# Performance work log

Measured on AMD Instinct MI355X. Metric: run time of the kernel, lower is better.

Reference implementation:

```python
import jax, jax.numpy as jnp
import numpy as np

N = 100000      # nodes
E = 1600000     # edges (avg degree 16)
F_IN = 128
F_OUT = 128
EPS = 1e-5      # BatchNorm eps


def setup_inputs() -> dict:
    key = jax.random.key(0)
    ks = jax.random.split(key, 10)
    s_in = 1.0 / np.sqrt(F_IN)
    s_out = 1.0 / np.sqrt(F_OUT)
    return {
        "x": jax.random.normal(ks[0], (N, F_IN), dtype=jnp.float32),
        "edge_index": jax.random.randint(ks[1], (2, E), 0, N, dtype=jnp.int32),
        # layer 0: SAGEConv(F_IN, F_OUT, aggr='max'); lin_l has bias, lin_r does not
        "W0_l": jax.random.normal(ks[2], (F_IN, F_OUT), dtype=jnp.float32) * s_in,
        "b0_l": jnp.zeros((F_OUT,), dtype=jnp.float32),
        "W0_r": jax.random.normal(ks[3], (F_IN, F_OUT), dtype=jnp.float32) * s_in,
        "gamma0": jnp.ones((F_OUT,), dtype=jnp.float32),
        "beta0": jnp.zeros((F_OUT,), dtype=jnp.float32),
        # layer 1: SAGEConv(F_OUT, F_OUT, aggr='max')
        "W1_l": jax.random.normal(ks[4], (F_OUT, F_OUT), dtype=jnp.float32) * s_out,
        "b1_l": jnp.zeros((F_OUT,), dtype=jnp.float32),
        "W1_r": jax.random.normal(ks[5], (F_OUT, F_OUT), dtype=jnp.float32) * s_out,
        "gamma1": jnp.ones((F_OUT,), dtype=jnp.float32),
        "beta1": jnp.zeros((F_OUT,), dtype=jnp.float32),
    }


def _sage_conv_max(x, src, dst, W_l, b_l, W_r):
    # gather source features along edges, scatter-max into destination nodes
    msgs = x[src]                                             # [E, F]
    agg = jax.ops.segment_max(msgs, dst, num_segments=N)      # [N, F], -inf for isolated
    agg = jnp.where(jnp.isfinite(agg), agg, 0.0)              # PyG fills empty segments with 0
    return agg @ W_l + b_l + x @ W_r                          # lin_l(aggr) + lin_r(x)


def _batch_norm(h, gamma, beta):
    mu = jnp.mean(h, axis=0)
    var = jnp.var(h, axis=0)
    return (h - mu) * jax.lax.rsqrt(var + EPS) * gamma + beta


def reference(x, edge_index, W0_l, b0_l, W0_r, gamma0, beta0,
              W1_l, b1_l, W1_r, gamma1, beta1):
    src, dst = edge_index[0], edge_index[1]
    h = _sage_conv_max(x, src, dst, W0_l, b0_l, W0_r)
    h = jax.nn.relu(_batch_norm(h, gamma0, beta0))
    h = _sage_conv_max(h, src, dst, W1_l, b1_l, W1_r)
    h = jax.nn.relu(_batch_norm(h, gamma1, beta1))
    return h
```

## Files before the change

kernel.cpp:

```cpp
#include <hip/hip_runtime.h>
#include <stdint.h>

#define EPS_BN 1e-5f

typedef __attribute__((ext_vector_type(8))) short short8v;
typedef __attribute__((ext_vector_type(4))) float f32x4;

__device__ __forceinline__ unsigned rne_bf16(float f) {
    unsigned u = __float_as_uint(f);
    return (u + 0x7FFFu + ((u >> 16) & 1u)) >> 16;
}

extern "C" __global__ __launch_bounds__(256)
void prep_kernel(const float4* __restrict__ x, uint2* __restrict__ x16, long n4, int cvB,
                 const float* __restrict__ Wl0, const float* __restrict__ Wr0,
                 unsigned short* __restrict__ Wt0,
                 const float* __restrict__ Wl1, const float* __restrict__ Wr1,
                 unsigned short* __restrict__ Wt1,
                 int* __restrict__ head, int Nn) {
    int b = blockIdx.x;
    if (b < cvB) {
        long i = (long)b * 256 + threadIdx.x;
        long stride = (long)cvB * 256;
        for (; i < n4; i += stride) {
            float4 v = x[i];
            uint2 o;
            o.x = rne_bf16(v.x) | (rne_bf16(v.y) << 16);
            o.y = rne_bf16(v.z) | (rne_bf16(v.w) << 16);
            x16[i] = o;
        }
    } else if (b < cvB + 256) {
        int wb = b - cvB;
        const float* Wl = (wb < 128) ? Wl0 : Wl1;
        const float* Wr = (wb < 128) ? Wr0 : Wr1;
        unsigned short* Wt = (wb < 128) ? Wt0 : Wt1;
        int idx = (wb & 127) * 256 + threadIdx.x;
        int col = idx >> 8, k = idx & 255;
        float v = (k < 128) ? Wl[(size_t)k * 128 + col]
                            : Wr[(size_t)(k - 128) * 128 + col];
        Wt[(size_t)col * 256 + k] = (unsigned short)rne_bf16(v);
    } else {
        int i = (b - cvB - 256) * 256 + threadIdx.x;
        if (i < Nn) head[i] = -1;
    }
}

extern "C" __global__ __launch_bounds__(256)
void link_kernel(const int* __restrict__ ei, int* __restrict__ head,
                 uint2* __restrict__ pair, int E) {
    int e = blockIdx.x * 256 + threadIdx.x;
    if (e < E) {
        int src = ei[e];
        int dst = ei[E + e];
        int old = atomicExch(&head[dst], e);
        uint2 p; p.x = (unsigned)src; p.y = (unsigned)old;
        pair[e] = p;
    }
}

extern "C" __global__ __launch_bounds__(256, 8)
void gather_max_ll16_kernel(const uint4* __restrict__ x16r, const int* __restrict__ head,
                            const uint2* __restrict__ pair,
                            uint4* __restrict__ agg16, float* __restrict__ stats, int Nn) {
    if (blockIdx.x == 0 && threadIdx.x < 256) stats[threadIdx.x] = 0.0f;
    int t = blockIdx.x * 256 + threadIdx.x;
    int node = t >> 4;
    if (node >= Nn) return;
    int lane = t & 15;
    int e = head[node];
    uint4 out;
    if (e >= 0) {
        uint2 p = pair[e];
        uint4 r = x16r[(size_t)p.x * 16 + lane];
        float a0 = __uint_as_float(r.x << 16), a1 = __uint_as_float(r.x);
        float a2 = __uint_as_float(r.y << 16), a3 = __uint_as_float(r.y);
        float a4 = __uint_as_float(r.z << 16), a5 = __uint_as_float(r.z);
        float a6 = __uint_as_float(r.w << 16), a7 = __uint_as_float(r.w);
        int en = (int)p.y;
        while (en >= 0) {
            uint2 pn = pair[en];
            uint4 v = x16r[(size_t)pn.x * 16 + lane];
            en = (int)pn.y;
            a0 = fmaxf(a0, __uint_as_float(v.x << 16));
            a1 = fmaxf(a1, __uint_as_float(v.x));
            a2 = fmaxf(a2, __uint_as_float(v.y << 16));
            a3 = fmaxf(a3, __uint_as_float(v.y));
            a4 = fmaxf(a4, __uint_as_float(v.z << 16));
            a5 = fmaxf(a5, __uint_as_float(v.z));
            a6 = fmaxf(a6, __uint_as_float(v.w << 16));
            a7 = fmaxf(a7, __uint_as_float(v.w));
        }
        out.x = (__float_as_uint(a0) >> 16) | (__float_as_uint(a1) & 0xFFFF0000u);
        out.y = (__float_as_uint(a2) >> 16) | (__float_as_uint(a3) & 0xFFFF0000u);
        out.z = (__float_as_uint(a4) >> 16) | (__float_as_uint(a5) & 0xFFFF0000u);
        out.w = (__float_as_uint(a6) >> 16) | (__float_as_uint(a7) & 0xFFFF0000u);
    } else {
        out.x = out.y = out.z = out.w = 0u;
    }
    agg16[(size_t)node * 16 + lane] = out;
}

extern "C" __global__ __launch_bounds__(256, 8)
void gather_max_bn_kernel(const uint4* __restrict__ h1r, const int* __restrict__ head,
                          const uint2* __restrict__ pair,
                          const float* __restrict__ stats0,
                          const float* __restrict__ gamma, const float* __restrict__ beta,
                          float inv_n,
                          uint4* __restrict__ agg16, uint4* __restrict__ y16,
                          float* __restrict__ stats1, int Nn) {
    __shared__ float scT[8][17];
    __shared__ float shT[8][17];
    {
        int t = threadIdx.x;
        if (t < 128) {
            float mu = stats0[t] * inv_n;
            float var = stats0[128 + t] * inv_n - mu * mu;
            float sc = gamma[t] * rsqrtf(var + EPS_BN);
            scT[t & 7][t >> 3] = sc;
            shT[t & 7][t >> 3] = beta[t] - mu * sc;
        }
        __syncthreads();
    }
    if (blockIdx.x == 0 && threadIdx.x < 256) stats1[threadIdx.x] = 0.0f;

    int t = blockIdx.x * 256 + threadIdx.x;
    int node = t >> 4;
    if (node >= Nn) return;
    int lane = t & 15;

    float sc[8], sh[8];
#pragma unroll
    for (int j = 0; j < 8; ++j) {
        sc[j] = scT[j][lane];
        sh[j] = shT[j][lane];
    }

    {
        uint4 r = h1r[(size_t)node * 16 + lane];
        float v0 = __uint_as_float(r.x << 16), v1 = __uint_as_float(r.x & 0xFFFF0000u);
        float v2 = __uint_as_float(r.y << 16), v3 = __uint_as_float(r.y & 0xFFFF0000u);
        float v4 = __uint_as_float(r.z << 16), v5 = __uint_as_float(r.z & 0xFFFF0000u);
        float v6 = __uint_as_float(r.w << 16), v7 = __uint_as_float(r.w & 0xFFFF0000u);
        v0 = fmaxf(fmaf(v0, sc[0], sh[0]), 0.f);
        v1 = fmaxf(fmaf(v1, sc[1], sh[1]), 0.f);
        v2 = fmaxf(fmaf(v2, sc[2], sh[2]), 0.f);
        v3 = fmaxf(fmaf(v3, sc[3], sh[3]), 0.f);
        v4 = fmaxf(fmaf(v4, sc[4], sh[4]), 0.f);
        v5 = fmaxf(fmaf(v5, sc[5], sh[5]), 0.f);
        v6 = fmaxf(fmaf(v6, sc[6], sh[6]), 0.f);
        v7 = fmaxf(fmaf(v7, sc[7], sh[7]), 0.f);
        uint4 o;
        o.x = rne_bf16(v0) | (rne_bf16(v1) << 16);
        o.y = rne_bf16(v2) | (rne_bf16(v3) << 16);
        o.z = rne_bf16(v4) | (rne_bf16(v5) << 16);
        o.w = rne_bf16(v6) | (rne_bf16(v7) << 16);
        y16[(size_t)node * 16 + lane] = o;
    }

    int e = head[node];
    uint4 out;
    if (e >= 0) {
        uint2 p = pair[e];
        uint4 r = h1r[(size_t)p.x * 16 + lane];
        float a0 = __uint_as_float(r.x << 16), a1 = __uint_as_float(r.x);
        float a2 = __uint_as_float(r.y << 16), a3 = __uint_as_float(r.y);
        float a4 = __uint_as_float(r.z << 16), a5 = __uint_as_float(r.z);
        float a6 = __uint_as_float(r.w << 16), a7 = __uint_as_float(r.w);
        int en = (int)p.y;
        while (en >= 0) {
            uint2 pn = pair[en];
            uint4 v = h1r[(size_t)pn.x * 16 + lane];
            en = (int)pn.y;
            a0 = fmaxf(a0, __uint_as_float(v.x << 16));
            a1 = fmaxf(a1, __uint_as_float(v.x));
            a2 = fmaxf(a2, __uint_as_float(v.y << 16));
            a3 = fmaxf(a3, __uint_as_float(v.y));
            a4 = fmaxf(a4, __uint_as_float(v.z << 16));
            a5 = fmaxf(a5, __uint_as_float(v.z));
            a6 = fmaxf(a6, __uint_as_float(v.w << 16));
            a7 = fmaxf(a7, __uint_as_float(v.w));
        }
        a1 = __uint_as_float(__float_as_uint(a1) & 0xFFFF0000u);
        a3 = __uint_as_float(__float_as_uint(a3) & 0xFFFF0000u);
        a5 = __uint_as_float(__float_as_uint(a5) & 0xFFFF0000u);
        a7 = __uint_as_float(__float_as_uint(a7) & 0xFFFF0000u);
        a0 = fmaxf(fmaf(a0, sc[0], sh[0]), 0.f);
        a1 = fmaxf(fmaf(a1, sc[1], sh[1]), 0.f);
        a2 = fmaxf(fmaf(a2, sc[2], sh[2]), 0.f);
        a3 = fmaxf(fmaf(a3, sc[3], sh[3]), 0.f);
        a4 = fmaxf(fmaf(a4, sc[4], sh[4]), 0.f);
        a5 = fmaxf(fmaf(a5, sc[5], sh[5]), 0.f);
        a6 = fmaxf(fmaf(a6, sc[6], sh[6]), 0.f);
        a7 = fmaxf(fmaf(a7, sc[7], sh[7]), 0.f);
        out.x = rne_bf16(a0) | (rne_bf16(a1) << 16);
        out.y = rne_bf16(a2) | (rne_bf16(a3) << 16);
        out.z = rne_bf16(a4) | (rne_bf16(a5) << 16);
        out.w = rne_bf16(a6) | (rne_bf16(a7) << 16);
    } else {
        out.x = out.y = out.z = out.w = 0u;
    }
    agg16[(size_t)node * 16 + lane] = out;
}

template <int OUT_BF16>
__device__ __forceinline__
void gemm_bf16_body(const unsigned short* __restrict__ agg16,
                    const unsigned short* __restrict__ xin16,
                    const unsigned short* __restrict__ Wt,
                    const float* __restrict__ bias,
                    void* __restrict__ hout, float* __restrict__ stats, int nrows) {
    __shared__ float redS[4][128];
    __shared__ float redQ[4][128];

    const int t = threadIdx.x;
    const int w = t >> 6, l = t & 63;
    const int wm = w >> 1, wn = w & 1;
    const int r16 = l & 15, g = l >> 4;
    const int blockRow = blockIdx.x * 128;
    const int colBase = wn * 64;

    f32x4 acc[4][4];
#pragma unroll
    for (int m = 0; m < 4; ++m)
#pragma unroll
        for (int n = 0; n < 4; ++n) acc[m][n] = (f32x4){0.f, 0.f, 0.f, 0.f};

    const short8v az = {0, 0, 0, 0, 0, 0, 0, 0};

#pragma unroll
    for (int kt = 0; kt < 8; ++kt) {
        const unsigned short* Asrc = (kt < 4) ? agg16 : xin16;
        const int kofs = (kt < 4) ? kt * 32 : kt * 32 - 128;

        short8v b[4];
#pragma unroll
        for (int n = 0; n < 4; ++n) {
            int col = colBase + n * 16 + r16;
            b[n] = *(const short8v*)(Wt + (size_t)col * 256 + kt * 32 + g * 8);
        }
        short8v a[4];
#pragma unroll
        for (int m = 0; m < 4; ++m) {
            int row = blockRow + wm * 64 + m * 16 + r16;
            a[m] = (row < nrows)
                 ? *(const short8v*)(Asrc + (size_t)row * 128 + kofs + g * 8)
                 : az;
        }
#pragma unroll
        for (int m = 0; m < 4; ++m)
#pragma unroll
            for (int n = 0; n < 4; ++n)
                acc[m][n] = __builtin_amdgcn_mfma_f32_16x16x32_bf16(a[m], b[n], acc[m][n], 0, 0, 0);
    }

    for (int i = t; i < 512; i += 256) {
        ((float*)redS)[i] = 0.f;
        ((float*)redQ)[i] = 0.f;
    }
    __syncthreads();

    float bcol[4];
#pragma unroll
    for (int n = 0; n < 4; ++n) bcol[n] = bias[colBase + n * 16 + r16];

    float s4[4] = {0.f, 0.f, 0.f, 0.f};
    float q4[4] = {0.f, 0.f, 0.f, 0.f};
#pragma unroll
    for (int m = 0; m < 4; ++m) {
#pragma unroll
        for (int reg = 0; reg < 4; ++reg) {
            int row = blockRow + wm * 64 + m * 16 + g * 4 + reg;
            if (row < nrows) {
#pragma unroll
                for (int n = 0; n < 4; ++n) {
                    float o = acc[m][n][reg] + bcol[n];
                    int col = colBase + n * 16 + r16;
                    if (OUT_BF16)
                        ((unsigned short*)hout)[(size_t)row * 128 + col] =
                            (unsigned short)rne_bf16(o);
                    else
                        ((float*)hout)[(size_t)row * 128 + col] = o;
                    s4[n] += o;
                    q4[n] += o * o;
                }
            }
        }
    }
#pragma unroll
    for (int n = 0; n < 4; ++n) {
        s4[n] += __shfl_xor(s4[n], 16, 64);
        s4[n] += __shfl_xor(s4[n], 32, 64);
        q4[n] += __shfl_xor(q4[n], 16, 64);
        q4[n] += __shfl_xor(q4[n], 32, 64);
    }
    if (g == 0) {
#pragma unroll
        for (int n = 0; n < 4; ++n) {
            redS[w][colBase + n * 16 + r16] = s4[n];
            redQ[w][colBase + n * 16 + r16] = q4[n];
        }
    }
    __syncthreads();
    if (t < 128) {
        float s = redS[0][t] + redS[1][t] + redS[2][t] + redS[3][t];
        float q = redQ[0][t] + redQ[1][t] + redQ[2][t] + redQ[3][t];
        atomicAdd(&stats[t], s);
        atomicAdd(&stats[128 + t], q);
    }
}

extern "C" __global__ __launch_bounds__(256)
void gemm_bf16_out16_kernel(const unsigned short* __restrict__ agg16,
                            const unsigned short* __restrict__ xin16,
                            const unsigned short* __restrict__ Wt,
                            const float* __restrict__ bias,
                            unsigned short* __restrict__ h, float* __restrict__ stats,
                            int nrows) {
    gemm_bf16_body<1>(agg16, xin16, Wt, bias, h, stats, nrows);
}

extern "C" __global__ __launch_bounds__(256)
void gemm_bf16_out32_kernel(const unsigned short* __restrict__ agg16,
                            const unsigned short* __restrict__ xin16,
                            const unsigned short* __restrict__ Wt,
                            const float* __restrict__ bias,
                            float* __restrict__ h, float* __restrict__ stats,
                            int nrows) {
    gemm_bf16_body<0>(agg16, xin16, Wt, bias, h, stats, nrows);
}

extern "C" __global__ __launch_bounds__(256)
void bn_relu_f32_kernel(float4* __restrict__ h, const float* __restrict__ stats,
                        const float* __restrict__ gamma, const float* __restrict__ beta,
                        float inv_n, long n4) {
    __shared__ float s_ss[256];
    {
        int t = threadIdx.x;
        if (t < 128) {
            float mu = stats[t] * inv_n;
            float var = stats[128 + t] * inv_n - mu * mu;
            float sc = gamma[t] * rsqrtf(var + EPS_BN);
            s_ss[t] = sc;
            s_ss[128 + t] = beta[t] - mu * sc;
        }
        __syncthreads();
    }
    long i = (long)blockIdx.x * blockDim.x + threadIdx.x;
    long stride = (long)gridDim.x * blockDim.x;
    for (; i < n4; i += stride) {
        int c4 = (int)(i & 31) * 4;
        float4 v = h[i];
        v.x = fmaxf(fmaf(v.x, s_ss[c4 + 0], s_ss[128 + c4 + 0]), 0.f);
        v.y = fmaxf(fmaf(v.y, s_ss[c4 + 1], s_ss[128 + c4 + 1]), 0.f);
        v.z = fmaxf(fmaf(v.z, s_ss[c4 + 2], s_ss[128 + c4 + 2]), 0.f);
        v.w = fmaxf(fmaf(v.w, s_ss[c4 + 3], s_ss[128 + c4 + 3]), 0.f);
        h[i] = v;
    }
}

__device__ __forceinline__ unsigned map_f(float f) {
    unsigned u = __float_as_uint(f);
    return (u & 0x80000000u) ? ~u : (u | 0x80000000u);
}
__device__ __forceinline__ float unmap_f(unsigned m) {
    return (m & 0x80000000u) ? __uint_as_float(m & 0x7FFFFFFFu) : __uint_as_float(~m);
}

extern "C" __global__ __launch_bounds__(256)
void init_sentinel_kernel(uint4* __restrict__ agg, long n4) {
    uint4 z = {0u, 0u, 0u, 0u};
    long i = (long)blockIdx.x * blockDim.x + threadIdx.x;
    long stride = (long)gridDim.x * blockDim.x;
    for (; i < n4; i += stride) agg[i] = z;
}

extern "C" __global__ __launch_bounds__(256)
void scatter_max_kernel(const float4* __restrict__ xin, const int* __restrict__ ei,
                        unsigned* __restrict__ agg, int E) {
    int t = blockIdx.x * 256 + threadIdx.x;
    int e = t >> 5;
    if (e >= E) return;
    int f4 = t & 31;
    int src = ei[e];
    int dst = ei[E + e];
    float4 v = xin[(size_t)src * 32 + f4];
    unsigned* p = agg + (size_t)dst * 128 + (size_t)f4 * 4;
    atomicMax(p + 0, map_f(v.x));
    atomicMax(p + 1, map_f(v.y));
    atomicMax(p + 2, map_f(v.z));
    atomicMax(p + 3, map_f(v.w));
}

extern "C" __global__ __launch_bounds__(256)
void unmap_kernel(unsigned* __restrict__ agg, long n) {
    long i = (long)blockIdx.x * blockDim.x + threadIdx.x;
    long stride = (long)gridDim.x * blockDim.x;
    for (; i < n; i += stride) {
        unsigned u = agg[i];
        agg[i] = __float_as_uint(u ? unmap_f(u) : 0.0f);
    }
}

extern "C" __global__
void zero_stats_kernel(float* __restrict__ stats) {
    stats[threadIdx.x] = 0.0f;
}

extern "C" __global__ __launch_bounds__(256)
void gemm_kernel(const float* __restrict__ agg, const float* __restrict__ xin,
                 const float* __restrict__ Wl, const float* __restrict__ Wr,
                 const float* __restrict__ bias, float* __restrict__ h,
                 float* __restrict__ stats, int nrows) {
    __shared__ __align__(16) float As[64][36];
    __shared__ __align__(16) float Bs[32][136];
    __shared__ float redS[4][128];
    __shared__ float redQ[4][128];

    const int t = threadIdx.x;
    const int tx = t & 15;
    const int ty = t >> 4;
    const int tx8 = tx * 8;
    const int ty4 = ty * 4;
    const int blockRow = blockIdx.x * 64;

    float acc[4][8];
#pragma unroll
    for (int j = 0; j < 4; ++j)
#pragma unroll
        for (int c = 0; c < 8; ++c) acc[j][c] = 0.0f;

    for (int kt = 0; kt < 8; ++kt) {
        const int k0 = kt * 32;
        const bool isAgg = (kt < 4);
        const float* W = isAgg ? Wl : Wr;
        const float* Asrc = isAgg ? agg : xin;
        const int kw = isAgg ? k0 : (k0 - 128);

#pragma unroll
        for (int it = 0; it < 4; ++it) {
            int idx = t + it * 256;
            int kr = idx >> 5, cq = idx & 31;
            float4 ww = *(const float4*)&W[(size_t)(kw + kr) * 128 + cq * 4];
            *(float4*)&Bs[kr][cq * 4] = ww;
        }
#pragma unroll
        for (int it = 0; it < 2; ++it) {
            int idx = t + it * 256;
            int r = idx >> 3, kq = idx & 7;
            int row_g = blockRow + r;
            float4 a = {0.f, 0.f, 0.f, 0.f};
            if (row_g < nrows)
                a = *(const float4*)&Asrc[(size_t)row_g * 128 + kw + kq * 4];
            *(float4*)&As[r][kq * 4] = a;
        }
        __syncthreads();

#pragma unroll
        for (int kk = 0; kk < 32; ++kk) {
            float aa[4];
            aa[0] = As[ty4 + 0][kk];
            aa[1] = As[ty4 + 1][kk];
            aa[2] = As[ty4 + 2][kk];
            aa[3] = As[ty4 + 3][kk];
            float4 b0 = *(const float4*)&Bs[kk][tx8];
            float4 b1 = *(const float4*)&Bs[kk][tx8 + 4];
            float bb[8] = {b0.x, b0.y, b0.z, b0.w, b1.x, b1.y, b1.z, b1.w};
#pragma unroll
            for (int j = 0; j < 4; ++j)
#pragma unroll
                for (int c = 0; c < 8; ++c)
                    acc[j][c] = fmaf(aa[j], bb[c], acc[j][c]);
        }
        __syncthreads();
    }

    float bv[8];
#pragma unroll
    for (int c = 0; c < 8; ++c) bv[c] = bias[tx8 + c];

    float s_loc[8], q_loc[8];
#pragma unroll
    for (int c = 0; c < 8; ++c) { s_loc[c] = 0.f; q_loc[c] = 0.f; }

#pragma unroll
    for (int j = 0; j < 4; ++j) {
        int row = blockRow + ty4 + j;
        if (row < nrows) {
            float o[8];
#pragma unroll
            for (int c = 0; c < 8; ++c) {
                o[c] = acc[j][c] + bv[c];
                s_loc[c] += o[c];
                q_loc[c] += o[c] * o[c];
            }
            float4 o0 = {o[0], o[1], o[2], o[3]};
            float4 o1 = {o[4], o[5], o[6], o[7]};
            *(float4*)&h[(size_t)row * 128 + tx8] = o0;
            *(float4*)&h[(size_t)row * 128 + tx8 + 4] = o1;
        }
    }

#pragma unroll
    for (int c = 0; c < 8; ++c) {
        s_loc[c] += __shfl_xor(s_loc[c], 16, 64);
        s_loc[c] += __shfl_xor(s_loc[c], 32, 64);
        q_loc[c] += __shfl_xor(q_loc[c], 16, 64);
        q_loc[c] += __shfl_xor(q_loc[c], 32, 64);
    }
    int wave = t >> 6;
    if ((t & 63) < 16) {
#pragma unroll
        for (int c = 0; c < 8; ++c) {
            redS[wave][tx8 + c] = s_loc[c];
            redQ[wave][tx8 + c] = q_loc[c];
        }
    }
    __syncthreads();
    if (t < 128) {
        float s = redS[0][t] + redS[1][t] + redS[2][t] + redS[3][t];
        float q = redQ[0][t] + redQ[1][t] + redQ[2][t] + redQ[3][t];
        atomicAdd(&stats[t], s);
        atomicAdd(&stats[128 + t], q);
    }
}

static void run_layer_atomic(const float* in_feat, const int* ei, int Nn, int Ee,
                             const float* Wl, const float* bl, const float* Wr,
                             const float* gamma, const float* beta,
                             float* agg, float* stats, float* out, hipStream_t stream) {
    long aggN = (long)Nn * 128;
    long n4 = aggN / 4;

    zero_stats_kernel<<<1, 256, 0, stream>>>(stats);
    int initBlocks = (int)((n4 + 255) / 256);
    if (initBlocks > 4096) initBlocks = 4096;
    init_sentinel_kernel<<<initBlocks, 256, 0, stream>>>((uint4*)agg, n4);
    int sb = (int)(((long)Ee * 32 + 255) / 256);
    scatter_max_kernel<<<sb, 256, 0, stream>>>((const float4*)in_feat, ei,
                                               (unsigned*)agg, Ee);
    int ub = (int)((aggN + 255) / 256);
    if (ub > 8192) ub = 8192;
    unmap_kernel<<<ub, 256, 0, stream>>>((unsigned*)agg, aggN);
    gemm_kernel<<<(Nn + 63) / 64, 256, 0, stream>>>(agg, in_feat, Wl, Wr, bl,
                                                    out, stats, Nn);
    int bnBlocks = (int)((n4 + 255) / 256);
    if (bnBlocks > 8192) bnBlocks = 8192;
    bn_relu_f32_kernel<<<bnBlocks, 256, 0, stream>>>((float4*)out, stats, gamma, beta,
                                                     1.0f / (float)Nn, n4);
}

extern "C" void kernel_launch(void* const* d_in, const int* in_sizes, int n_in,
                              void* d_out, int out_size, void* d_ws, size_t ws_size,
                              hipStream_t stream) {
    (void)n_in; (void)out_size;
    const float* x     = (const float*)d_in[0];
    const int*   ei    = (const int*)d_in[1];
    const float* W0_l  = (const float*)d_in[2];
    const float* b0_l  = (const float*)d_in[3];
    const float* W0_r  = (const float*)d_in[4];
    const float* g0    = (const float*)d_in[5];
    const float* be0   = (const float*)d_in[6];
    const float* W1_l  = (const float*)d_in[7];
    const float* b1_l  = (const float*)d_in[8];
    const float* W1_r  = (const float*)d_in[9];
    const float* g1    = (const float*)d_in[10];
    const float* be1   = (const float*)d_in[11];

    int Nn = in_sizes[0] / 128;
    int Ee = in_sizes[1] / 2;
    long n4 = (long)Nn * 32;
    float inv_n = 1.0f / (float)Nn;

    char* p = (char*)d_ws;
    unsigned short* xy16 = (unsigned short*)p;  p += (size_t)Nn * 128 * 2;
    unsigned short* agg16 = (unsigned short*)p; p += (size_t)Nn * 128 * 2;
    float* stats0 = (float*)p;                  p += 256 * sizeof(float);
    float* stats1 = (float*)p;                  p += 256 * sizeof(float);
    unsigned short* Wt0 = (unsigned short*)p;   p += 128 * 256 * 2;
    unsigned short* Wt1 = (unsigned short*)p;   p += 128 * 256 * 2;
    int* head = (int*)p;                        p += (size_t)Nn * sizeof(int);
    uint2* pair = (uint2*)p;                    p += (size_t)Ee * sizeof(uint2);
    size_t needed = (size_t)(p - (char*)d_ws);
    float* out = (float*)d_out;
    unsigned short* h1 = (unsigned short*)d_out;

    if (ws_size >= needed) {
        int cvB = (int)((n4 + 255) / 256);
        if (cvB > 4096) cvB = 4096;
        int hB = (Nn + 255) / 256;
        prep_kernel<<<cvB + 256 + hB, 256, 0, stream>>>(
            (const float4*)x, (uint2*)xy16, n4, cvB,
            W0_l, W0_r, Wt0, W1_l, W1_r, Wt1, head, Nn);
        link_kernel<<<(Ee + 255) / 256, 256, 0, stream>>>(ei, head, pair, Ee);

        int gB = (Nn * 16 + 255) / 256;
        int mB = (Nn + 127) / 128;
        int bnB = (int)((n4 + 255) / 256);
        if (bnB > 8192) bnB = 8192;

        gather_max_ll16_kernel<<<gB, 256, 0, stream>>>(
            (const uint4*)xy16, head, pair, (uint4*)agg16, stats0, Nn);
        gemm_bf16_out16_kernel<<<mB, 256, 0, stream>>>(agg16, xy16, Wt0, b0_l,
                                                       h1, stats0, Nn);
        gather_max_bn_kernel<<<gB, 256, 0, stream>>>(
            (const uint4*)h1, head, pair, stats0, g0, be0, inv_n,
            (uint4*)agg16, (uint4*)xy16, stats1, Nn);
        gemm_bf16_out32_kernel<<<mB, 256, 0, stream>>>(agg16, xy16, Wt1, b1_l,
                                                       out, stats1, Nn);
        bn_relu_f32_kernel<<<bnB, 256, 0, stream>>>((float4*)out, stats1, g1, be1,
                                                    inv_n, n4);
    } else {
        float* agg = (float*)d_ws;
        float* fstats = (float*)((char*)d_ws + (size_t)Nn * 128 * sizeof(float));
        run_layer_atomic(x, ei, Nn, Ee, W0_l, b0_l, W0_r, g0, be0,
                         agg, fstats, out, stream);
        run_layer_atomic(out, ei, Nn, Ee, W1_l, b1_l, W1_r, g1, be1,
                         agg, fstats, out, stream);
    }
}
```

Baseline: 393.4 us.

## Build CSR via degree histogram and scan so layer-2 gather uses contiguous source lists

Adds a degree histogram in the link kernel plus a three-kernel exclusive scan to form row offsets. The first-layer gather, while walking the linked list, writes each node's source indices into a contiguous CSR array. The second-layer gather then reads contiguous indices and issues two feature loads per iteration, removing the dependent pointer chase. The cost is three extra small launches, an extra atomic per edge and extra index writes in layer one.

```diff
diff --git a/kernel.cpp b/kernel.cpp
--- a/kernel.cpp
+++ b/kernel.cpp
@@ -17,7 +17,7 @@
                  unsigned short* __restrict__ Wt0,
                  const float* __restrict__ Wl1, const float* __restrict__ Wr1,
                  unsigned short* __restrict__ Wt1,
-                 int* __restrict__ head, int Nn) {
+                 int* __restrict__ head, int* __restrict__ deg, int Nn) {
     int b = blockIdx.x;
     if (b < cvB) {
         long i = (long)b * 256 + threadIdx.x;
@@ -41,13 +41,13 @@
         Wt[(size_t)col * 256 + k] = (unsigned short)rne_bf16(v);
     } else {
         int i = (b - cvB - 256) * 256 + threadIdx.x;
-        if (i < Nn) head[i] = -1;
-    }
-}
-
-extern "C" __global__ __launch_bounds__(256)
-void link_kernel(const int* __restrict__ ei, int* __restrict__ head,
-                 uint2* __restrict__ pair, int E) {
+        if (i < Nn) { head[i] = -1; deg[i] = 0; }
+    }
+}
+
+extern "C" __global__ __launch_bounds__(256)
+void link_hist_kernel(const int* __restrict__ ei, int* __restrict__ head,
+                      uint2* __restrict__ pair, int* __restrict__ deg, int E) {
     int e = blockIdx.x * 256 + threadIdx.x;
     if (e < E) {
         int src = ei[e];
@@ -55,12 +55,85 @@
         int old = atomicExch(&head[dst], e);
         uint2 p; p.x = (unsigned)src; p.y = (unsigned)old;
         pair[e] = p;
-    }
+        atomicAdd(&deg[dst], 1);
+    }
+}
+
+extern "C" __global__ __launch_bounds__(256)
+void block_sum_kernel(const int* __restrict__ deg, int* __restrict__ bsum, int Nn) {
+    __shared__ int tsum[256];
+    int t = threadIdx.x;
+    int base = blockIdx.x * 1024 + t * 4;
+    int s = 0;
+#pragma unroll
+    for (int j = 0; j < 4; ++j) {
+        int i = base + j;
+        if (i < Nn) s += deg[i];
+    }
+    tsum[t] = s;
+    __syncthreads();
+    for (int off = 128; off > 0; off >>= 1) {
+        if (t < off) tsum[t] += tsum[t + off];
+        __syncthreads();
+    }
+    if (t == 0) bsum[blockIdx.x] = tsum[0];
+}
+
+extern "C" __global__ __launch_bounds__(1024)
+void scan_bsums_kernel(const int* __restrict__ bsum, int* __restrict__ boff, int NB) {
+    __shared__ int sh[1024];
+    int t = threadIdx.x;
+    int v = (t < NB) ? bsum[t] : 0;
+    sh[t] = v;
+    __syncthreads();
+    for (int off = 1; off < 1024; off <<= 1) {
+        int add = (t >= off) ? sh[t - off] : 0;
+        __syncthreads();
+        sh[t] += add;
+        __syncthreads();
+    }
+    if (t < NB) boff[t] = sh[t] - v;
+}
+
+extern "C" __global__ __launch_bounds__(256)
+void scan_apply_kernel(const int* __restrict__ deg, const int* __restrict__ boff,
+                       int* __restrict__ row_start, int Nn) {
+    __shared__ int tsum[256];
+    int t = threadIdx.x;
+    int base = blockIdx.x * 1024 + t * 4;
+    int v[4];
+    int s = 0;
+#pragma unroll
+    for (int j = 0; j < 4; ++j) {
+        int i = base + j;
+        v[j] = (i < Nn) ? deg[i] : 0;
+        s += v[j];
+    }
+    tsum[t] = s;
+    __syncthreads();
+    for (int off = 1; off < 256; off <<= 1) {
+        int add = (t >= off) ? tsum[t - off] : 0;
+        __syncthreads();
+        tsum[t] += add;
+        __syncthreads();
+    }
+    int run = boff[blockIdx.x] + (t ? tsum[t - 1] : 0);
+#pragma unroll
+    for (int j = 0; j < 4; ++j) {
+        int i = base + j;
+        if (i < Nn) {
+            row_start[i] = run;
+            run += v[j];
+        }
+    }
+    if (blockIdx.x == gridDim.x - 1 && t == 255)
+        row_start[Nn] = boff[blockIdx.x] + tsum[255];
 }
 
 extern "C" __global__ __launch_bounds__(256, 8)
 void gather_max_ll16_kernel(const uint4* __restrict__ x16r, const int* __restrict__ head,
                             const uint2* __restrict__ pair,
+                            const int* __restrict__ row_start, int* __restrict__ ssrc,
                             uint4* __restrict__ agg16, float* __restrict__ stats, int Nn) {
     if (blockIdx.x == 0 && threadIdx.x < 256) stats[threadIdx.x] = 0.0f;
     int t = blockIdx.x * 256 + threadIdx.x;
@@ -70,7 +143,10 @@
     int e = head[node];
     uint4 out;
     if (e >= 0) {
+        int wp = row_start[node];
         uint2 p = pair[e];
+        if (lane == 0) ssrc[wp] = (int)p.x;
+        ++wp;
         uint4 r = x16r[(size_t)p.x * 16 + lane];
         float a0 = __uint_as_float(r.x << 16), a1 = __uint_as_float(r.x);
         float a2 = __uint_as_float(r.y << 16), a3 = __uint_as_float(r.y);
@@ -79,6 +155,8 @@
         int en = (int)p.y;
         while (en >= 0) {
             uint2 pn = pair[en];
+            if (lane == 0) ssrc[wp] = (int)pn.x;
+            ++wp;
             uint4 v = x16r[(size_t)pn.x * 16 + lane];
             en = (int)pn.y;
             a0 = fmaxf(a0, __uint_as_float(v.x << 16));
@@ -100,14 +178,25 @@
     agg16[(size_t)node * 16 + lane] = out;
 }
 
+#define FM8A(v)                                             \
+    a0 = fmaxf(a0, __uint_as_float((v).x << 16));           \
+    a1 = fmaxf(a1, __uint_as_float((v).x));                 \
+    a2 = fmaxf(a2, __uint_as_float((v).y << 16));           \
+    a3 = fmaxf(a3, __uint_as_float((v).y));                 \
+    a4 = fmaxf(a4, __uint_as_float((v).z << 16));           \
+    a5 = fmaxf(a5, __uint_as_float((v).z));                 \
+    a6 = fmaxf(a6, __uint_as_float((v).w << 16));           \
+    a7 = fmaxf(a7, __uint_as_float((v).w));
+
 extern "C" __global__ __launch_bounds__(256, 8)
-void gather_max_bn_kernel(const uint4* __restrict__ h1r, const int* __restrict__ head,
-                          const uint2* __restrict__ pair,
-                          const float* __restrict__ stats0,
-                          const float* __restrict__ gamma, const float* __restrict__ beta,
-                          float inv_n,
-                          uint4* __restrict__ agg16, uint4* __restrict__ y16,
-                          float* __restrict__ stats1, int Nn) {
+void gather_max_bn_csr_kernel(const uint4* __restrict__ h1r,
+                              const int* __restrict__ row_start,
+                              const int* __restrict__ ssrc,
+                              const float* __restrict__ stats0,
+                              const float* __restrict__ gamma,
+                              const float* __restrict__ beta, float inv_n,
+                              uint4* __restrict__ agg16, uint4* __restrict__ y16,
+                              float* __restrict__ stats1, int Nn) {
     __shared__ float scT[8][17];
     __shared__ float shT[8][17];
     {
@@ -157,28 +246,30 @@
         y16[(size_t)node * 16 + lane] = o;
     }
 
-    int e = head[node];
+    int beg = row_start[node];
+    int end = row_start[node + 1];
     uint4 out;
-    if (e >= 0) {
-        uint2 p = pair[e];
-        uint4 r = h1r[(size_t)p.x * 16 + lane];
+    if (beg < end) {
+        int s0 = ssrc[beg];
+        uint4 r = h1r[(size_t)s0 * 16 + lane];
         float a0 = __uint_as_float(r.x << 16), a1 = __uint_as_float(r.x);
         float a2 = __uint_as_float(r.y << 16), a3 = __uint_as_float(r.y);
         float a4 = __uint_as_float(r.z << 16), a5 = __uint_as_float(r.z);
         float a6 = __uint_as_float(r.w << 16), a7 = __uint_as_float(r.w);
-        int en = (int)p.y;
-        while (en >= 0) {
-            uint2 pn = pair[en];
-            uint4 v = h1r[(size_t)pn.x * 16 + lane];
-            en = (int)pn.y;
-            a0 = fmaxf(a0, __uint_as_float(v.x << 16));
-            a1 = fmaxf(a1, __uint_as_float(v.x));
-            a2 = fmaxf(a2, __uint_as_float(v.y << 16));
-            a3 = fmaxf(a3, __uint_as_float(v.y));
-            a4 = fmaxf(a4, __uint_as_float(v.z << 16));
-            a5 = fmaxf(a5, __uint_as_float(v.z));
-            a6 = fmaxf(a6, __uint_as_float(v.w << 16));
-            a7 = fmaxf(a7, __uint_as_float(v.w));
+        int i = beg + 1;
+        if (((end - beg) & 1) == 0 && i < end) {
+            int s = ssrc[i];
+            uint4 v = h1r[(size_t)s * 16 + lane];
+            FM8A(v);
+            ++i;
+        }
+        for (; i < end; i += 2) {
+            int sa = ssrc[i];
+            int sb = ssrc[i + 1];
+            uint4 va = h1r[(size_t)sa * 16 + lane];
+            uint4 vb = h1r[(size_t)sb * 16 + lane];
+            FM8A(va);
+            FM8A(vb);
         }
         a1 = __uint_as_float(__float_as_uint(a1) & 0xFFFF0000u);
         a3 = __uint_as_float(__float_as_uint(a3) & 0xFFFF0000u);
@@ -570,6 +661,7 @@
     int Ee = in_sizes[1] / 2;
     long n4 = (long)Nn * 32;
     float inv_n = 1.0f / (float)Nn;
+    int NB = (Nn + 1023) / 1024;
 
     char* p = (char*)d_ws;
     unsigned short* xy16 = (unsigned short*)p;  p += (size_t)Nn * 128 * 2;
@@ -579,19 +671,27 @@
     unsigned short* Wt0 = (unsigned short*)p;   p += 128 * 256 * 2;
     unsigned short* Wt1 = (unsigned short*)p;   p += 128 * 256 * 2;
     int* head = (int*)p;                        p += (size_t)Nn * sizeof(int);
+    int* deg = (int*)p;                         p += (size_t)Nn * sizeof(int);
+    int* row_start = (int*)p;                   p += (size_t)(Nn + 1) * sizeof(int);
+    int* bsum = (int*)p;                        p += (size_t)NB * sizeof(int);
+    int* boff = (int*)p;                        p += (size_t)NB * sizeof(int);
     uint2* pair = (uint2*)p;                    p += (size_t)Ee * sizeof(uint2);
+    int* ssrc = (int*)p;                        p += (size_t)Ee * sizeof(int);
     size_t needed = (size_t)(p - (char*)d_ws);
     float* out = (float*)d_out;
     unsigned short* h1 = (unsigned short*)d_out;
 
-    if (ws_size >= needed) {
+    if (ws_size >= needed && NB <= 1024) {
         int cvB = (int)((n4 + 255) / 256);
         if (cvB > 4096) cvB = 4096;
         int hB = (Nn + 255) / 256;
         prep_kernel<<<cvB + 256 + hB, 256, 0, stream>>>(
             (const float4*)x, (uint2*)xy16, n4, cvB,
-            W0_l, W0_r, Wt0, W1_l, W1_r, Wt1, head, Nn);
-        link_kernel<<<(Ee + 255) / 256, 256, 0, stream>>>(ei, head, pair, Ee);
+            W0_l, W0_r, Wt0, W1_l, W1_r, Wt1, head, deg, Nn);
+        link_hist_kernel<<<(Ee + 255) / 256, 256, 0, stream>>>(ei, head, pair, deg, Ee);
+        block_sum_kernel<<<NB, 256, 0, stream>>>(deg, bsum, Nn);
+        scan_bsums_kernel<<<1, 1024, 0, stream>>>(bsum, boff, NB);
+        scan_apply_kernel<<<NB, 256, 0, stream>>>(deg, boff, row_start, Nn);
 
         int gB = (Nn * 16 + 255) / 256;
         int mB = (Nn + 127) / 128;
@@ -599,11 +699,12 @@
         if (bnB > 8192) bnB = 8192;
 
         gather_max_ll16_kernel<<<gB, 256, 0, stream>>>(
-            (const uint4*)xy16, head, pair, (uint4*)agg16, stats0, Nn);
+            (const uint4*)xy16, head, pair, row_start, ssrc,
+            (uint4*)agg16, stats0, Nn);
         gemm_bf16_out16_kernel<<<mB, 256, 0, stream>>>(agg16, xy16, Wt0, b0_l,
                                                        h1, stats0, Nn);
-        gather_max_bn_kernel<<<gB, 256, 0, stream>>>(
-            (const uint4*)h1, head, pair, stats0, g0, be0, inv_n,
+        gather_max_bn_csr_kernel<<<gB, 256, 0, stream>>>(
+            (const uint4*)h1, row_start, ssrc, stats0, g0, be0, inv_n,
             (uint4*)agg16, (uint4*)xy16, stats1, Nn);
         gemm_bf16_out32_kernel<<<mB, 256, 0, stream>>>(agg16, xy16, Wt1, b1_l,
                                                        out, stats1, Nn);
```

After: 463.5 us. +17.8%, slower.
